# Kernel optimization log

Hardware: AMD Instinct MI355X
Metric: run time of the kernel (lower is better)

## Reference

```python
import jax, jax.numpy as jnp
import numpy as np

RESO = 64
VSIZE = 0.3
VOXEL = VSIZE / RESO
HALF = VOXEL / 2.0


def _voxel_xyz():
    line = (np.arange(RESO, dtype=np.float32) * VOXEL + HALF)
    x, y, z = np.meshgrid(line, line, line, indexing='ij')
    return jnp.asarray(np.stack([x, y, z]))  # [3,R,R,R]


def _grid_sample_2d(feats, gx, gy):
    # feats: [NV,C,H,W]; gx,gy: [NV,N] normalized coords (torch align_corners-style)
    NV, C, H, W = feats.shape
    ix = (gx + 1.0) * 0.5 * (W - 1)
    iy = (gy + 1.0) * 0.5 * (H - 1)
    ix0 = jnp.floor(ix); iy0 = jnp.floor(iy)
    ix1 = ix0 + 1.0;     iy1 = iy0 + 1.0
    # bilinear weights from unclamped corners
    w_nw = (ix1 - ix) * (iy1 - iy)
    w_ne = (ix - ix0) * (iy1 - iy)
    w_sw = (ix1 - ix) * (iy - iy0)
    w_se = (ix - ix0) * (iy - iy0)
    mask = ((ix >= 0) & (ix <= W - 1) & (iy >= 0) & (iy <= H - 1)).astype(feats.dtype)
    cx0 = jnp.clip(ix0, 0, W - 1).astype(jnp.int32)
    cx1 = jnp.clip(ix1, 0, W - 1).astype(jnp.int32)
    cy0 = jnp.clip(iy0, 0, H - 1).astype(jnp.int32)
    cy1 = jnp.clip(iy1, 0, H - 1).astype(jnp.int32)
    feats_flat = feats.reshape(NV, C, H * W)  # [NV,C,HW]
    gather = jax.vmap(lambda f, i: f[:, i])   # per-view [C,HW],[N] -> [C,N]
    v_nw = gather(feats_flat, cy0 * W + cx0)
    v_ne = gather(feats_flat, cy0 * W + cx1)
    v_sw = gather(feats_flat, cy1 * W + cx0)
    v_se = gather(feats_flat, cy1 * W + cx1)
    out = (v_nw * w_nw[:, None] + v_ne * w_ne[:, None]
           + v_sw * w_sw[:, None] + v_se * w_se[:, None])  # [NV,C,N]
    return out, mask


def setup_inputs() -> dict:
    key = jax.random.key(0)
    k_feat, k1, k2, k3 = jax.random.split(key, 4)
    NV, C, H, W = 8, 32, 128, 128
    feats = jax.random.normal(k_feat, (NV, C, H, W), dtype=jnp.float32)
    # realistic pinhole intrinsics for a 512x512 image
    K = np.array([[400.0, 0.0, 256.0], [0.0, 400.0, 256.0], [0.0, 0.0, 1.0]], np.float32)
    Ks = jnp.asarray(np.tile(K, (NV, 1, 1)))
    # identity-rotation w2c poses, camera ~0.5m from volume along +z
    poses = []
    for i in range(NV):
        t = np.array([0.02 * (i - 3.5), 0.01 * (i % 2), 0.5 + 0.02 * i], np.float32)
        poses.append(np.concatenate([np.eye(3, dtype=np.float32), t[:, None]], axis=1))
    ref_poses = jnp.asarray(np.stack(poses))
    bbox = jnp.asarray(np.array([[-0.15, -0.15, 0.0], [0.15, 0.15, 0.3]], np.float32))
    W1 = jax.random.normal(k1, (32, 32), dtype=jnp.float32) * 0.1
    W2 = jax.random.normal(k2, (32, 16), dtype=jnp.float32) * 0.1
    W3 = jax.random.normal(k3, (16, 8), dtype=jnp.float32) * 0.1
    return {"feats": feats, "ref_poses": ref_poses, "Ks": Ks, "bbox": bbox,
            "img_h": 512, "img_w": 512,
            "W1": W1, "b1": jnp.zeros((32,), jnp.float32),
            "W2": W2, "b2": jnp.zeros((16,), jnp.float32),
            "W3": W3, "b3": jnp.zeros((8,), jnp.float32)}


def reference(feats, ref_poses, Ks, bbox, img_h, img_w, W1, b1, W2, b2, W3, b3):
    NV, C, H, W = feats.shape
    dt = feats.dtype
    # homogeneous pad of poses and intrinsics
    pose_h = jnp.tile(jnp.eye(4, dtype=dt), (NV, 1, 1)).at[:, :3, :4].set(ref_poses)
    K_pad = jnp.tile(jnp.eye(4, dtype=dt), (NV, 1, 1)).at[:, :3, :3].set(Ks)
    w2pixel = K_pad @ pose_h  # [NV,4,4]
    # voxel centers in world frame
    xyz = _voxel_xyz() + bbox[0][:, None, None, None]  # [3,R,R,R]
    pts = xyz.reshape(3, -1)                            # [3,N], N=R^3
    homo = jnp.concatenate([pts, jnp.ones_like(pts[0:1])], axis=0)  # [4,N]
    pix = jnp.einsum('vij,jn->vin', w2pixel, homo)[:, :3]           # [NV,3,N]
    z = pix[:, 2]                                                    # [NV,N]
    mask_valid_depth = (z > 0).astype(dt)
    uv = pix[:, :2] / z[:, None, :]                                  # [NV,2,N]
    normalizer = jnp.array([img_w, img_h], dtype=dt)
    grid = uv.transpose(0, 2, 1) / normalizer - 1.0                  # [NV,N,2]
    feat, mask = _grid_sample_2d(feats, grid[..., 0], grid[..., 1])  # [NV,C,N],[NV,N]
    mask = mask * mask_valid_depth
    # [NV,C,(X Y Z)] -> [NV,X,Y,Z,C]
    feat = feat.transpose(0, 2, 1).reshape(NV, RESO, RESO, RESO, C)
    mask = mask.reshape(NV, RESO, RESO, RESO)
    # NOTE: original normalizes over dim=1 (NumX), replicated faithfully
    weight = mask / (jnp.sum(mask, axis=1, keepdims=True) + 1e-8)
    weight = weight[..., None]  # [NV,R,R,R,1]
    h1 = jax.nn.relu(feat @ W1 + b1)
    h2 = jax.nn.relu(h1 @ W2 + b2)
    comp = h2 @ W3 + b3  # [NV,R,R,R,8]
    mean = jnp.sum(comp * weight, axis=0, keepdims=True)
    var = jnp.sum(weight * (comp - mean) ** 2, axis=0, keepdims=True)
    mv = jnp.concatenate([mean, var], axis=-1)       # [1,R,R,R,16]
    return jnp.transpose(mv, (0, 4, 3, 2, 1))        # [1,16,Z,Y,X]
```

## Files before the change

### kernel.cpp

```cpp
#include <hip/hip_runtime.h>
#include <math.h>

#define NVIEW 8
#define CIN   32
#define HF    128
#define WF    128
#define C1    32
#define C2    16
#define C3    8
#define RESO  64
#define PLANE (HF*WF)

typedef _Float16 half8_t  __attribute__((ext_vector_type(8)));
typedef _Float16 half2_t  __attribute__((ext_vector_type(2)));
typedef float    floatx4  __attribute__((ext_vector_type(4)));

static __device__ __forceinline__ float vox_coord(int idx, float b) {
    const float VOXEL = (float)(0.3 / 64.0);
    const float HALFV = (float)(0.3 / 128.0);
    return (float)idx * VOXEL + HALFV + b;
}

static __device__ __forceinline__ void wave_lds_sync() {
    asm volatile("s_waitcnt lgkmcnt(0)" ::: "memory");
}

__global__ void __launch_bounds__(256) k_g(const float* __restrict__ feats,
                                           const float* __restrict__ W1,
                                           const float* __restrict__ b1,
                                           uint4* __restrict__ Gh,
                                           const float* __restrict__ Ks,
                                           const float* __restrict__ poses,
                                           const int* __restrict__ ihp,
                                           const int* __restrict__ iwp,
                                           const float* __restrict__ W2,
                                           const float* __restrict__ b2,
                                           const float* __restrict__ W3,
                                           const float* __restrict__ b3,
                                           float* __restrict__ mats,
                                           _Float16* __restrict__ w2f,
                                           _Float16* __restrict__ w3f,
                                           float* __restrict__ b2f,
                                           float* __restrict__ b3f) {
    if (blockIdx.x == 512) {
        int t = threadIdx.x;
        if (t < NVIEW * 12) {
            int v = t / 12, rc = t % 12, r = rc / 4, c = rc % 4;
            const float* K = Ks + v * 9;
            const float* P = poses + v * 12;
            float s = K[r*3+0]*P[0*4+c] + K[r*3+1]*P[1*4+c] + K[r*3+2]*P[2*4+c];
            float sc = (r == 0) ? 63.5f / (float)iwp[0]
                     : (r == 1) ? 63.5f / (float)ihp[0] : 1.0f;
            mats[v*12 + r*4 + c] = s * sc;
        }
        if (t < 64) {
            int n = t & 15, g = t >> 4;
#pragma unroll
            for (int jj = 0; jj < 8; jj++) {
                int kk = 8 * g + jj;
                w2f[t*8 + jj] = (_Float16)W2[kk * C2 + n];
                float w3v = (kk < C2 && n < C3) ? W3[kk * C3 + n] : 0.0f;
                w3f[t*8 + jj] = (_Float16)w3v;
            }
            b2f[t] = b2[n];
            b3f[t] = (n < C3) ? b3[n] : 0.0f;
        }
        return;
    }
    int bx = blockIdx.x;
    int pix = (bx & 63) * 256 + threadIdx.x;
    int v   = bx >> 6;
    const float* fp = feats + ((size_t)v * CIN) * PLANE + pix;
    float g[32];
#pragma unroll
    for (int o = 0; o < C1; o++) g[o] = b1[o];
#pragma unroll
    for (int cc = 0; cc < CIN; cc += 8) {
        float fc[8];
#pragma unroll
        for (int q = 0; q < 8; q++) fc[q] = fp[(size_t)(cc + q) * PLANE];
#pragma unroll
        for (int q = 0; q < 8; q++) {
#pragma unroll
            for (int o = 0; o < C1; o++)
                g[o] = fmaf(fc[q], W1[(cc + q) * C1 + o], g[o]);
        }
    }
#pragma unroll
    for (int grp = 0; grp < 4; grp++) {
        union { half2_t h2[4]; uint4 u; } pk;
#pragma unroll
        for (int q = 0; q < 4; q++) {
            half2_t p = { (_Float16)g[grp*8 + 2*q], (_Float16)g[grp*8 + 2*q + 1] };
            pk.h2[q] = p;
        }
        Gh[((size_t)(v * 4 + grp)) * PLANE + pix] = pk.u;
    }
}

__global__ void __launch_bounds__(256, 4) k_main(
    const uint4* __restrict__ Gh,
    const float* __restrict__ mats, const float* __restrict__ bbox,
    const _Float16* __restrict__ w2f, const _Float16* __restrict__ w3f,
    const float* __restrict__ b2f, const float* __restrict__ b3f,
    float* __restrict__ out) {
#pragma clang fp contract(fast)
    __shared__ __align__(16) _Float16 h2s[4][64 * 24];

    int tid  = threadIdx.x;
    int wv   = tid >> 6;
    int lane = tid & 63;
    int bxs  = (blockIdx.x & 7) * 128 + (blockIdx.x >> 3);
    int col  = bxs * 4 + wv;
    int j  = col & 63;
    int kz = col >> 6;
    _Float16* h2b = h2s[wv];

    int m = lane & 15, g = lane >> 4;
    float y = vox_coord(j, bbox[1]);
    float z = vox_coord(kz, bbox[2]);

    half8_t w2frag = *(const half8_t*)(w2f + lane * 8);
    half8_t w3frag = *(const half8_t*)(w3f + lane * 8);
    float b2c = b2f[lane];
    float b3c = b3f[lane];
    floatx4 cb2 = {b2c, b2c, b2c, b2c};
    floatx4 cb3 = {b3c, b3c, b3c, b3c};
    const half2_t z2 = { (_Float16)0.0f, (_Float16)0.0f };

    float M1[16], Msq[16], S16[16];
#pragma unroll
    for (int c = 0; c < 16; c++) { M1[c] = 0.0f; Msq[c] = 0.0f; S16[c] = 0.0f; }

#pragma unroll 2
    for (int v = 0; v < NVIEW; v++) {
        const float* M = mats + v * 12;
        const uint4* Gv = Gh + (size_t)(v * 4 + g) * PLANE;

        float Ku = fmaf(M[1], y, fmaf(M[2],  z, M[3]));
        float Kv = fmaf(M[5], y, fmaf(M[6],  z, M[7]));
        float Kz = fmaf(M[9], y, fmaf(M[10], z, M[11]));
        float M0 = M[0], M4 = M[4], M8 = M[8];

        floatx4 c2v[4];
        unsigned int ballo[4];
        int popc = 0;

#pragma unroll
        for (int T = 0; T < 4; T++) {
            int ipt = T * 16 + m;
            float x = vox_coord(ipt, bbox[0]);
            float u  = fmaf(M0, x, Ku);
            float vv = fmaf(M4, x, Kv);
            float zc = fmaf(M8, x, Kz);
            float invz = __builtin_amdgcn_rcpf(zc);
            float ix = u * invz;
            float iy = vv * invz;

            float fx0 = floorf(ix), fy0 = floorf(iy);
            float fx1 = fx0 + 1.0f, fy1 = fy0 + 1.0f;
            bool inb = (ix >= 0.0f) && (ix <= (float)(WF-1)) &&
                       (iy >= 0.0f) && (iy <= (float)(HF-1)) && (zc > 0.0f);
            int cx0 = (int)fminf(fmaxf(fx0, 0.0f), (float)(WF-1));
            int cx1 = (int)fminf(fmaxf(fx1, 0.0f), (float)(WF-1));
            int cy0 = (int)fminf(fmaxf(fy0, 0.0f), (float)(HF-1));
            int cy1 = (int)fminf(fmaxf(fy1, 0.0f), (float)(HF-1));
            float wnw = (fx1 - ix) * (fy1 - iy);
            float wne = (ix - fx0) * (fy1 - iy);
            float wsw = (fx1 - ix) * (iy - fy0);
            float wse = (ix - fx0) * (iy - fy0);

            unsigned long long bal = __ballot(inb);
            ballo[T] = (unsigned int)bal;
            popc += __popcll(bal);

            int t00 = cy0 * WF + cx0, t01 = cy0 * WF + cx1;
            int t10 = cy1 * WF + cx0, t11 = cy1 * WF + cx1;
            uint4 A = Gv[t00], B = Gv[t01], C = Gv[t10], D = Gv[t11];

            half2_t wnw2 = { (_Float16)wnw, (_Float16)wnw };
            half2_t wne2 = { (_Float16)wne, (_Float16)wne };
            half2_t wsw2 = { (_Float16)wsw, (_Float16)wsw };
            half2_t wse2 = { (_Float16)wse, (_Float16)wse };

            union { uint4 u; half2_t h[4]; } ua, ub, uc, ud;
            ua.u = A; ub.u = B; uc.u = C; ud.u = D;
            union { half2_t h2[4]; half8_t h8; } r;
#pragma unroll
            for (int c = 0; c < 4; c++) {
                half2_t e = ua.h[c]*wnw2 + ub.h[c]*wne2 + uc.h[c]*wsw2 + ud.h[c]*wse2;
                r.h2[c] = __builtin_elementwise_max(e, z2);
            }

            c2v[T] = __builtin_amdgcn_mfma_f32_16x16x32_f16(r.h8, w2frag, cb2, 0, 0, 0);
        }

        wave_lds_sync();
#pragma unroll
        for (int T = 0; T < 4; T++) {
#pragma unroll
            for (int r = 0; r < 4; r++) {
                float vv = fmaxf(c2v[T][r], 0.0f);
                h2b[(T*16 + g*4 + r) * 24 + m] = (_Float16)vv;
            }
        }
        wave_lds_sync();

        float msr = __builtin_amdgcn_rcpf((float)(popc >> 2) + 1e-8f);
#pragma unroll
        for (int T = 0; T < 4; T++) {
            half8_t a3 = *(const half8_t*)(h2b + (T*16 + m) * 24 + (g & 1) * 8);
            floatx4 c3 = __builtin_amdgcn_mfma_f32_16x16x32_f16(a3, w3frag, cb3, 0, 0, 0);
#pragma unroll
            for (int r = 0; r < 4; r++) {
                float w = ((ballo[T] >> (g*4 + r)) & 1u) ? msr : 0.0f;
                float val = c3[r];
                float t1 = w * val;
                S16[T*4+r] += w;
                M1[T*4+r]  += t1;
                Msq[T*4+r]  = fmaf(t1, val, Msq[T*4+r]);
            }
        }
    }

    if (m < C3) {
        size_t base = (size_t)col * 64;
#pragma unroll
        for (int T = 0; T < 4; T++) {
            float4 mn, vr;
            mn.x = M1[T*4+0]; mn.y = M1[T*4+1]; mn.z = M1[T*4+2]; mn.w = M1[T*4+3];
            vr.x = fmaf(mn.x*mn.x, S16[T*4+0]-2.0f, Msq[T*4+0]);
            vr.y = fmaf(mn.y*mn.y, S16[T*4+1]-2.0f, Msq[T*4+1]);
            vr.z = fmaf(mn.z*mn.z, S16[T*4+2]-2.0f, Msq[T*4+2]);
            vr.w = fmaf(mn.w*mn.w, S16[T*4+3]-2.0f, Msq[T*4+3]);
            size_t ob = base + T*16 + g*4;
            *(float4*)(out + (size_t)m       * 262144 + ob) = mn;
            *(float4*)(out + (size_t)(m + 8) * 262144 + ob) = vr;
        }
    }
}

extern "C" void kernel_launch(void* const* d_in, const int* in_sizes, int n_in,
                              void* d_out, int out_size, void* d_ws, size_t ws_size,
                              hipStream_t stream) {
    const float* feats = (const float*)d_in[0];
    const float* poses = (const float*)d_in[1];
    const float* Ks    = (const float*)d_in[2];
    const float* bbox  = (const float*)d_in[3];
    const int*   img_h = (const int*)d_in[4];
    const int*   img_w = (const int*)d_in[5];
    const float* W1    = (const float*)d_in[6];
    const float* b1    = (const float*)d_in[7];
    const float* W2    = (const float*)d_in[8];
    const float* b2    = (const float*)d_in[9];
    const float* W3    = (const float*)d_in[10];
    const float* b3    = (const float*)d_in[11];
    float* out = (float*)d_out;
    float* ws  = (float*)d_ws;

    float*     mats = ws;
    _Float16*  w2f  = (_Float16*)(ws + 128);
    _Float16*  w3f  = (_Float16*)(ws + 384);
    float*     b2f  = ws + 640;
    float*     b3f  = ws + 704;
    uint4*     Gh   = (uint4*)(ws + 768);

    hipLaunchKernelGGL(k_g, dim3(513), dim3(256), 0, stream,
                       feats, W1, b1, Gh, Ks, poses, img_h, img_w,
                       W2, b2, W3, b3, mats, w2f, w3f, b2f, b3f);
    hipLaunchKernelGGL(k_main, dim3(1024), dim3(256), 0, stream,
                       Gh, mats, bbox, w2f, w3f, b2f, b3f, out);
}
```

Before: 130.2 us.

## Interleave G channels per pixel and sample one voxel per lane

Changes the precomputed G buffer layout from channel-group planes to 64 contiguous bytes per pixel, so each lane fetches all 32 channels of its bilinear corners with four 16-byte loads. Each lane now handles one x-voxel instead of four lanes sharing a voxel across channel groups. This removes redundant projection math and spreads the corner reads over contiguous lines. In exchange the blended features go through a swizzled LDS staging buffer before the layer-2 MFMA, which adds LDS traffic and a wave sync. The view loop is no longer unrolled.

```diff
diff --git a/kernel.cpp b/kernel.cpp
--- a/kernel.cpp
+++ b/kernel.cpp
@@ -86,6 +86,7 @@
                 g[o] = fmaf(fc[q], W1[(cc + q) * C1 + o], g[o]);
         }
     }
+    uint4* gp = Gh + ((size_t)v * PLANE + pix) * 4;
 #pragma unroll
     for (int grp = 0; grp < 4; grp++) {
         union { half2_t h2[4]; uint4 u; } pk;
@@ -94,7 +95,7 @@
             half2_t p = { (_Float16)g[grp*8 + 2*q], (_Float16)g[grp*8 + 2*q + 1] };
             pk.h2[q] = p;
         }
-        Gh[((size_t)(v * 4 + grp)) * PLANE + pix] = pk.u;
+        gp[grp] = pk.u;
     }
 }
 
@@ -105,6 +106,7 @@
     const float* __restrict__ b2f, const float* __restrict__ b3f,
     float* __restrict__ out) {
 #pragma clang fp contract(fast)
+    __shared__ __align__(16) _Float16 a2s[4][64 * 32];
     __shared__ __align__(16) _Float16 h2s[4][64 * 24];
 
     int tid  = threadIdx.x;
@@ -114,11 +116,13 @@
     int col  = bxs * 4 + wv;
     int j  = col & 63;
     int kz = col >> 6;
+    _Float16* a2b = a2s[wv];
     _Float16* h2b = h2s[wv];
 
     int m = lane & 15, g = lane >> 4;
     float y = vox_coord(j, bbox[1]);
     float z = vox_coord(kz, bbox[2]);
+    float x = vox_coord(lane, bbox[0]);
 
     half8_t w2frag = *(const half8_t*)(w2f + lane * 8);
     half8_t w3frag = *(const half8_t*)(w3f + lane * 8);
@@ -128,92 +132,108 @@
     floatx4 cb3 = {b3c, b3c, b3c, b3c};
     const half2_t z2 = { (_Float16)0.0f, (_Float16)0.0f };
 
+    int wsw0 = (lane >> 1) & 3;
+    int rsw0 = (m >> 1) & 3;
+
     float M1[16], Msq[16], S16[16];
 #pragma unroll
     for (int c = 0; c < 16; c++) { M1[c] = 0.0f; Msq[c] = 0.0f; S16[c] = 0.0f; }
 
-#pragma unroll 2
+#pragma unroll 1
     for (int v = 0; v < NVIEW; v++) {
         const float* M = mats + v * 12;
-        const uint4* Gv = Gh + (size_t)(v * 4 + g) * PLANE;
+        const uint4* Gp = Gh + (size_t)v * (PLANE * 4);
 
         float Ku = fmaf(M[1], y, fmaf(M[2],  z, M[3]));
         float Kv = fmaf(M[5], y, fmaf(M[6],  z, M[7]));
         float Kz = fmaf(M[9], y, fmaf(M[10], z, M[11]));
-        float M0 = M[0], M4 = M[4], M8 = M[8];
-
-        floatx4 c2v[4];
-        unsigned int ballo[4];
-        int popc = 0;
+
+        float u  = fmaf(M[0], x, Ku);
+        float vv = fmaf(M[4], x, Kv);
+        float zc = fmaf(M[8], x, Kz);
+        float invz = __builtin_amdgcn_rcpf(zc);
+        float ix = u * invz;
+        float iy = vv * invz;
+
+        float fx0 = floorf(ix), fy0 = floorf(iy);
+        float fx1 = fx0 + 1.0f, fy1 = fy0 + 1.0f;
+        bool inb = (ix >= 0.0f) && (ix <= (float)(WF-1)) &&
+                   (iy >= 0.0f) && (iy <= (float)(HF-1)) && (zc > 0.0f);
+        int cx0 = (int)fminf(fmaxf(fx0, 0.0f), (float)(WF-1));
+        int cx1 = (int)fminf(fmaxf(fx1, 0.0f), (float)(WF-1));
+        int cy0 = (int)fminf(fmaxf(fy0, 0.0f), (float)(HF-1));
+        int cy1 = (int)fminf(fmaxf(fy1, 0.0f), (float)(HF-1));
+        float wnw = (fx1 - ix) * (fy1 - iy);
+        float wne = (ix - fx0) * (fy1 - iy);
+        float wsw = (fx1 - ix) * (iy - fy0);
+        float wse = (ix - fx0) * (iy - fy0);
+
+        unsigned long long bal = __ballot(inb);
+        int popc = __popcll(bal);
+
+        int t00 = cy0 * WF + cx0, t01 = cy0 * WF + cx1;
+        int t10 = cy1 * WF + cx0, t11 = cy1 * WF + cx1;
+        const uint4* pA = Gp + (size_t)t00 * 4;
+        const uint4* pB = Gp + (size_t)t01 * 4;
+        const uint4* pC = Gp + (size_t)t10 * 4;
+        const uint4* pD = Gp + (size_t)t11 * 4;
+
+        half2_t wnw2 = { (_Float16)wnw, (_Float16)wnw };
+        half2_t wne2 = { (_Float16)wne, (_Float16)wne };
+        half2_t wsw2 = { (_Float16)wsw, (_Float16)wsw };
+        half2_t wse2 = { (_Float16)wse, (_Float16)wse };
+
+        union { uint4 u[4]; half2_t h[16]; } ca, cb, cc4, cd, acc;
+#pragma unroll
+        for (int q = 0; q < 4; q++) ca.u[q] = pA[q];
+#pragma unroll
+        for (int q = 0; q < 4; q++) cb.u[q] = pB[q];
+#pragma unroll
+        for (int c = 0; c < 16; c++) acc.h[c] = ca.h[c] * wnw2;
+#pragma unroll
+        for (int q = 0; q < 4; q++) cc4.u[q] = pC[q];
+#pragma unroll
+        for (int c = 0; c < 16; c++) acc.h[c] = cb.h[c] * wne2 + acc.h[c];
+#pragma unroll
+        for (int q = 0; q < 4; q++) cd.u[q] = pD[q];
+#pragma unroll
+        for (int c = 0; c < 16; c++) acc.h[c] = cc4.h[c] * wsw2 + acc.h[c];
+#pragma unroll
+        for (int c = 0; c < 16; c++) {
+            acc.h[c] = cd.h[c] * wse2 + acc.h[c];
+            acc.h[c] = __builtin_elementwise_max(acc.h[c], z2);
+        }
+
+#pragma unroll
+        for (int q = 0; q < 4; q++)
+            *(uint4*)(a2b + lane * 32 + (q ^ wsw0) * 8) = acc.u[q];
+        wave_lds_sync();
 
 #pragma unroll
         for (int T = 0; T < 4; T++) {
-            int ipt = T * 16 + m;
-            float x = vox_coord(ipt, bbox[0]);
-            float u  = fmaf(M0, x, Ku);
-            float vv = fmaf(M4, x, Kv);
-            float zc = fmaf(M8, x, Kz);
-            float invz = __builtin_amdgcn_rcpf(zc);
-            float ix = u * invz;
-            float iy = vv * invz;
-
-            float fx0 = floorf(ix), fy0 = floorf(iy);
-            float fx1 = fx0 + 1.0f, fy1 = fy0 + 1.0f;
-            bool inb = (ix >= 0.0f) && (ix <= (float)(WF-1)) &&
-                       (iy >= 0.0f) && (iy <= (float)(HF-1)) && (zc > 0.0f);
-            int cx0 = (int)fminf(fmaxf(fx0, 0.0f), (float)(WF-1));
-            int cx1 = (int)fminf(fmaxf(fx1, 0.0f), (float)(WF-1));
-            int cy0 = (int)fminf(fmaxf(fy0, 0.0f), (float)(HF-1));
-            int cy1 = (int)fminf(fmaxf(fy1, 0.0f), (float)(HF-1));
-            float wnw = (fx1 - ix) * (fy1 - iy);
-            float wne = (ix - fx0) * (fy1 - iy);
-            float wsw = (fx1 - ix) * (iy - fy0);
-            float wse = (ix - fx0) * (iy - fy0);
-
-            unsigned long long bal = __ballot(inb);
-            ballo[T] = (unsigned int)bal;
-            popc += __popcll(bal);
-
-            int t00 = cy0 * WF + cx0, t01 = cy0 * WF + cx1;
-            int t10 = cy1 * WF + cx0, t11 = cy1 * WF + cx1;
-            uint4 A = Gv[t00], B = Gv[t01], C = Gv[t10], D = Gv[t11];
-
-            half2_t wnw2 = { (_Float16)wnw, (_Float16)wnw };
-            half2_t wne2 = { (_Float16)wne, (_Float16)wne };
-            half2_t wsw2 = { (_Float16)wsw, (_Float16)wsw };
-            half2_t wse2 = { (_Float16)wse, (_Float16)wse };
-
-            union { uint4 u; half2_t h[4]; } ua, ub, uc, ud;
-            ua.u = A; ub.u = B; uc.u = C; ud.u = D;
-            union { half2_t h2[4]; half8_t h8; } r;
-#pragma unroll
-            for (int c = 0; c < 4; c++) {
-                half2_t e = ua.h[c]*wnw2 + ub.h[c]*wne2 + uc.h[c]*wsw2 + ud.h[c]*wse2;
-                r.h2[c] = __builtin_elementwise_max(e, z2);
+            half8_t a2 = *(const half8_t*)(a2b + (T*16 + m) * 32 + (g ^ rsw0) * 8);
+            floatx4 c2 = __builtin_amdgcn_mfma_f32_16x16x32_f16(a2, w2frag, cb2, 0, 0, 0);
+#pragma unroll
+            for (int r = 0; r < 4; r++) {
+                float hv = fmaxf(c2[r], 0.0f);
+                h2b[(T*16 + g*4 + r) * 24 + m] = (_Float16)hv;
             }
-
-            c2v[T] = __builtin_amdgcn_mfma_f32_16x16x32_f16(r.h8, w2frag, cb2, 0, 0, 0);
-        }
-
+        }
         wave_lds_sync();
-#pragma unroll
-        for (int T = 0; T < 4; T++) {
-#pragma unroll
-            for (int r = 0; r < 4; r++) {
-                float vv = fmaxf(c2v[T][r], 0.0f);
-                h2b[(T*16 + g*4 + r) * 24 + m] = (_Float16)vv;
-            }
-        }
-        wave_lds_sync();
-
-        float msr = __builtin_amdgcn_rcpf((float)(popc >> 2) + 1e-8f);
+
+        float msr = __builtin_amdgcn_rcpf((float)popc + 1e-8f);
+        unsigned int balT[4];
+        balT[0] = (unsigned int)bal;
+        balT[1] = (unsigned int)(bal >> 16);
+        balT[2] = (unsigned int)(bal >> 32);
+        balT[3] = (unsigned int)(bal >> 48);
 #pragma unroll
         for (int T = 0; T < 4; T++) {
             half8_t a3 = *(const half8_t*)(h2b + (T*16 + m) * 24 + (g & 1) * 8);
             floatx4 c3 = __builtin_amdgcn_mfma_f32_16x16x32_f16(a3, w3frag, cb3, 0, 0, 0);
 #pragma unroll
             for (int r = 0; r < 4; r++) {
-                float w = ((ballo[T] >> (g*4 + r)) & 1u) ? msr : 0.0f;
+                float w = ((balT[T] >> (g*4 + r)) & 1u) ? msr : 0.0f;
                 float val = c3[r];
                 float t1 = w * val;
                 S16[T*4+r] += w;
```

After: 128.4 us. No clear change (-1.3%).
